# Optimization experiments

Measured on AMD Instinct MI355X. Metric: run time of the kernel, lower is better.

## Reference

```python
import jax, jax.numpy as jnp
import numpy as np

B, N, T, D, H, K = 16, 64, 32, 512, 256, 13
S = N * T  # flattened document length
PAD_TAG = 0


def setup_inputs():
    key = jax.random.key(0)
    ks = jax.random.split(key, 16)
    x = jax.random.normal(ks[0], (B, N, T, D), jnp.float32)
    x_gcn = jax.random.normal(ks[1], (B, N, D), jnp.float32)
    length = jax.random.randint(ks[2], (B, N), 1, T + 1)
    mask = (jnp.arange(T)[None, None, :] < length[:, :, None]).astype(jnp.int32)
    tags = jax.random.randint(ks[3], (B, N, T), 0, K)
    s = 0.05
    w_ih_f = jax.random.normal(ks[4], (4 * H, D), jnp.float32) * s
    w_hh_f = jax.random.normal(ks[5], (4 * H, H), jnp.float32) * s
    b_f = jax.random.normal(ks[6], (4 * H,), jnp.float32) * s
    w_ih_b = jax.random.normal(ks[7], (4 * H, D), jnp.float32) * s
    w_hh_b = jax.random.normal(ks[8], (4 * H, H), jnp.float32) * s
    b_b = jax.random.normal(ks[9], (4 * H,), jnp.float32) * s
    mlp_w = jax.random.normal(ks[10], (K, 2 * H), jnp.float32) * s
    mlp_b = jax.random.normal(ks[11], (K,), jnp.float32) * s
    transitions = jax.random.normal(ks[12], (K, K), jnp.float32) * s
    start_trans = jax.random.normal(ks[13], (K,), jnp.float32) * s
    end_trans = jax.random.normal(ks[14], (K,), jnp.float32) * s
    return dict(x=x, x_gcn=x_gcn, mask=mask, length=length, tags=tags,
                w_ih_f=w_ih_f, w_hh_f=w_hh_f, b_f=b_f,
                w_ih_b=w_ih_b, w_hh_b=w_hh_b, b_b=b_b,
                mlp_w=mlp_w, mlp_b=mlp_b,
                transitions=transitions, start_trans=start_trans, end_trans=end_trans)


def _pack_one(v, dest):
    # scatter valid rows to compacted positions; invalid rows land in dummy slot S
    out = jnp.zeros((S + 1,) + v.shape[1:], v.dtype).at[dest].set(v)
    return out[:S]


def union_layer(x, x_gcn, mask, length, tags):
    xf = x.reshape(B, S, D)
    mf = mask.reshape(B, S)
    tf = tags.reshape(B, S)
    doc_len = length.sum(-1)  # (B,)
    cum = jnp.cumsum(mf, axis=1)
    dest = jnp.where(mf == 1, cum - 1, S)  # invalid -> dummy slot
    new_x = jax.vmap(_pack_one)(xf, dest)
    new_tag = jax.vmap(_pack_one)(tf, dest)  # pad tag = 0
    new_mask = (jnp.arange(S)[None, :] < doc_len[:, None]).astype(mf.dtype)
    gcn_flat = jnp.broadcast_to(x_gcn[:, :, None, :], (B, N, T, D)).reshape(B, S, D)
    return gcn_flat + new_x, new_mask, doc_len, new_tag


def lstm_dir(xs, w_ih, w_hh, b):
    # xs: (B, S, Din) -> hidden states (B, S, H)
    def step(carry, xt):
        h, c = carry
        g = xt @ w_ih.T + h @ w_hh.T + b
        i, f, gg, o = jnp.split(g, 4, axis=-1)
        c = jax.nn.sigmoid(f) * c + jax.nn.sigmoid(i) * jnp.tanh(gg)
        h = jax.nn.sigmoid(o) * jnp.tanh(c)
        return (h, c), h
    init = (jnp.zeros((B, H), xs.dtype), jnp.zeros((B, H), xs.dtype))
    _, hs = jax.lax.scan(step, init, jnp.swapaxes(xs, 0, 1))
    return jnp.swapaxes(hs, 0, 1)


def bilstm(new_x, doc_len, w_ih_f, w_hh_f, b_f, w_ih_b, w_hh_b, b_b):
    t = jnp.arange(S)[None, :]
    L = doc_len[:, None]
    rev = jnp.where(t < L, L - 1 - t, t)  # per-sample reversal within valid region (involution)
    out_f = lstm_dir(new_x, w_ih_f, w_hh_f, b_f)
    x_rev = jnp.take_along_axis(new_x, rev[:, :, None], axis=1)
    out_b = lstm_dir(x_rev, w_ih_b, w_hh_b, b_b)
    out_b = jnp.take_along_axis(out_b, rev[:, :, None], axis=1)
    return jnp.concatenate([out_f, out_b], axis=-1)  # (B, S, 2H)


def crf_log_likelihood(logits, tags, mask, doc_len, transitions, start_trans, end_trans):
    maskf = mask.astype(logits.dtype)
    # numerator: score of the gold path
    emit = jnp.take_along_axis(logits, tags[:, :, None], axis=2)[..., 0]  # (B,S)
    num = start_trans[tags[:, 0]] + (emit * maskf).sum(1)
    tr = transitions[tags[:, :-1], tags[:, 1:]] * maskf[:, 1:]
    num = num + tr.sum(1)
    last_tag = jnp.take_along_axis(tags, (doc_len - 1)[:, None], axis=1)[:, 0]
    num = num + end_trans[last_tag]
    # denominator: forward algorithm
    alpha0 = start_trans[None, :] + logits[:, 0]
    def step(alpha, inp):
        e, m = inp  # (B,K), (B,)
        new = jax.nn.logsumexp(alpha[:, :, None] + transitions[None] + e[:, None, :], axis=1)
        return jnp.where(m[:, None] > 0, new, alpha), None
    alpha, _ = jax.lax.scan(step, alpha0,
                            (jnp.swapaxes(logits[:, 1:], 0, 1), jnp.swapaxes(mask[:, 1:], 0, 1)))
    log_z = jax.nn.logsumexp(alpha + end_trans[None, :], axis=-1)
    return num - log_z  # (B,) per-doc log-likelihood (keepdim=True)


def reference(x, x_gcn, mask, length, tags,
              w_ih_f, w_hh_f, b_f, w_ih_b, w_hh_b, b_b,
              mlp_w, mlp_b, transitions, start_trans, end_trans):
    new_x, new_mask, doc_len, new_tag = union_layer(x, x_gcn, mask, length, tags)
    out = bilstm(new_x, doc_len, w_ih_f, w_hh_f, b_f, w_ih_b, w_hh_b, b_b)
    out = out * new_mask[:, :, None].astype(out.dtype)  # packed-seq padding semantics
    logits = out @ mlp_w.T + mlp_b  # (B, S, K)
    ll = crf_log_likelihood(logits, new_tag, new_mask, doc_len,
                            transitions, start_trans, end_trans)
    return logits, new_mask, ll
```

## Files before the change

kernel.cpp:

```cpp
#include <hip/hip_runtime.h>
#include <hip/hip_fp16.h>
#include <hip/hip_bf16.h>

#define B_ 16
#define N_ 64
#define T_ 32
#define D_ 512
#define H_ 256
#define K_ 13
#define S_ 2048
#define G4_ 1024

typedef float f32x4 __attribute__((ext_vector_type(4)));
typedef short s16x8 __attribute__((ext_vector_type(8)));
typedef int   i32x4 __attribute__((ext_vector_type(4)));

#define INVQ 2.0505324e-5f

#define BAR() do { \
  asm volatile("s_waitcnt lgkmcnt(0)" ::: "memory"); \
  __builtin_amdgcn_s_barrier(); \
  __builtin_amdgcn_sched_barrier(0); \
} while (0)

__device__ __forceinline__ float sigm(float x){ return 1.0f/(1.0f+__expf(-x)); }
__device__ __forceinline__ float tanh_fast(float x){ return 1.0f - 2.0f/(1.0f+__expf(2.0f*x)); }

__global__ void k_prep(const int* __restrict__ length, int* __restrict__ cum, int* __restrict__ doc){
  const int b = threadIdx.x >> 6, n = threadIdx.x & 63;
  const int v = length[b*N_ + n];
  int x = v;
  #pragma unroll
  for (int d = 1; d < 64; d <<= 1){
    int y = __shfl_up(x, d);
    if (n >= d) x += y;
  }
  cum[b*N_ + n] = x - v;
  if (n == 63) doc[b] = x;
}

__global__ __launch_bounds__(256) void k_cast(const float* __restrict__ wf, const float* __restrict__ wb,
                       const float* __restrict__ hf, const float* __restrict__ hb,
                       ushort* __restrict__ wih, signed char* __restrict__ whh8){
  const int i = blockIdx.x*256 + threadIdx.x;
  if (i < 2*G4_*D_){
    const int dir = i / (G4_*D_); const int r = i % (G4_*D_);
    const float v = dir ? wb[r] : wf[r];
    ((__hip_bfloat16*)wih)[i] = __float2bfloat16(v);
  } else {
    const int j2 = i - 2*G4_*D_;
    if (j2 < 2*G4_*H_){
      const int dir = j2 >> 18; const int r = j2 & 262143;
      const float v = (dir ? hb : hf)[r];
      int q = (int)rintf(v * 384.0f);
      whh8[j2] = (signed char)min(127, max(-127, q));
    }
  }
}

__global__ __launch_bounds__(256) void k_srcmap(const int* __restrict__ length, const int* __restrict__ cum,
                         const int* __restrict__ tags, int* __restrict__ src, int* __restrict__ ntag){
  const int i = blockIdx.x*256 + threadIdx.x;
  const int b = i >> 11, nt = i & 2047, n = nt >> 5, t = nt & 31;
  if (t < length[b*N_ + n]){
    const int dest = cum[b*N_ + n] + t;
    src[b*S_ + dest] = nt;
    ntag[b*S_ + dest] = tags[i];
  }
}

__global__ __launch_bounds__(256) void k_newx(const float* __restrict__ x, const float* __restrict__ gcn,
                      const int* __restrict__ src, const int* __restrict__ doc,
                      ushort* __restrict__ nx, float* __restrict__ mask_out){
  const int r = blockIdx.x; const int b = r >> 11, s = r & 2047;
  const int L = doc[b];
  const int d = threadIdx.x*2;
  const float2 g2 = *(const float2*)&gcn[((size_t)(b*N_ + (s>>5)))*D_ + d];
  float v0 = g2.x, v1 = g2.y;
  if (s < L){
    const int nt = src[r];
    const float2 x2 = *(const float2*)&x[((size_t)(b*S_ + nt))*D_ + d];
    v0 += x2.x; v1 += x2.y;
  }
  __hip_bfloat16* o = (__hip_bfloat16*)nx + (size_t)r*D_ + d;
  o[0] = __float2bfloat16(v0); o[1] = __float2bfloat16(v1);
  if (threadIdx.x == 0) mask_out[r] = (s < L) ? 1.0f : 0.0f;
}

__global__ __launch_bounds__(256) void k_gemm(const ushort* __restrict__ A, const ushort* __restrict__ Bw,
    const float* __restrict__ bias_f, const float* __restrict__ bias_b,
    const int* __restrict__ doc, __half* __restrict__ pre){
  const int m0 = blockIdx.x*128, n0 = blockIdx.y*128;
  const int b = m0 >> 11, s0 = m0 & 2047;
  if (s0 >= doc[b]) return;
  __shared__ __align__(16) ushort la[128*40];
  __shared__ __align__(16) ushort lb[128*40];
  const int tid = threadIdx.x, lane = tid & 63, w = tid >> 6;
  const int wr = w >> 1, wc = w & 1;
  const int fr = lane & 15, fq = lane >> 4;
  f32x4 acc[4][4] = {};
  const int srow = tid >> 1;
  const int sko  = (tid & 1)*16;
  for (int kt = 0; kt < 16; ++kt){
    const int k0 = kt*32;
    const float4 a0 = *(const float4*)&A[(size_t)(m0+srow)*512 + k0 + sko];
    const float4 a1 = *(const float4*)&A[(size_t)(m0+srow)*512 + k0 + sko + 8];
    const float4 b0 = *(const float4*)&Bw[(size_t)(n0+srow)*512 + k0 + sko];
    const float4 b1 = *(const float4*)&Bw[(size_t)(n0+srow)*512 + k0 + sko + 8];
    *(float4*)&la[srow*40 + sko]     = a0;
    *(float4*)&la[srow*40 + sko + 8] = a1;
    *(float4*)&lb[srow*40 + sko]     = b0;
    *(float4*)&lb[srow*40 + sko + 8] = b1;
    __syncthreads();
    s16x8 af[4], bfr[4];
    #pragma unroll
    for (int mi=0; mi<4; ++mi) af[mi] = *(const s16x8*)&la[(wr*64+mi*16+fr)*40 + fq*8];
    #pragma unroll
    for (int ni=0; ni<4; ++ni) bfr[ni] = *(const s16x8*)&lb[(wc*64+ni*16+fr)*40 + fq*8];
    #pragma unroll
    for (int mi=0; mi<4; ++mi){
      #pragma unroll
      for (int ni=0; ni<4; ++ni){
        acc[mi][ni] = __builtin_amdgcn_mfma_f32_16x16x32_bf16(af[mi], bfr[ni], acc[mi][ni], 0, 0, 0);
      }
    }
    __syncthreads();
  }
  #pragma unroll
  for (int ni=0; ni<4; ++ni){
    const int n = n0 + wc*64 + ni*16 + fr;
    const float bv = (n < 1024) ? bias_f[n] : bias_b[n-1024];
    #pragma unroll
    for (int mi=0; mi<4; ++mi){
      const int mb = m0 + wr*64 + mi*16 + fq*4;
      #pragma unroll
      for (int j=0; j<4; ++j)
        pre[(size_t)(mb+j)*2048 + n] = __float2half(acc[mi][ni][j] + bv);
    }
  }
}

__global__ __launch_bounds__(512, 2) void k_recur4(
    const signed char* __restrict__ W8,
    const __half* __restrict__ pre, const int* __restrict__ doc,
    float* __restrict__ outh)
{
  const int b = blockIdx.x >> 1, dir = blockIdx.x & 1;
  const int tid = threadIdx.x, lane = tid & 63, wv = tid >> 6;
  const int L = doc[b];

  __shared__ __align__(16) unsigned char hq[2][256];
  __shared__ __align__(16) __half pls[2][1024];

  if (tid < 128) ((unsigned*)hq)[tid] = 0u;

  i32x4 wfrag[2][4][4];
  #pragma unroll
  for (int nt = 0; nt < 2; ++nt)
    #pragma unroll
    for (int g = 0; g < 4; ++g){
      const int row = g*256 + wv*32 + nt*16 + (lane & 15);
      #pragma unroll
      for (int kt = 0; kt < 4; ++kt)
        wfrag[nt][g][kt] = *(const i32x4*)&W8[(size_t)dir*262144 + (size_t)row*256 + kt*64 + (lane>>4)*16];
    }

  auto ldpre = [&](int tt){
    const int pos = dir ? max(L-1-tt, 0) : tt;
    return *(const unsigned*)(pre + ((size_t)(b*S_ + pos))*2048 + dir*1024 + tid*2);
  };

  const unsigned s0v = ldpre(0);
  unsigned f1 = (1 < L) ? ldpre(1) : 0u;
  unsigned f2 = (2 < L) ? ldpre(2) : 0u;
  *(unsigned*)((char*)&pls[0][0] + tid*4) = s0v;
  BAR();

  float cst = 0.f;
  const int u = wv*32 + (lane & 31);
  for (int t = 0; t < L; ++t){
    const int pcur = t & 1, pnxt = pcur ^ 1;
    const int rbuf = (t+1) & 1, wbuf = t & 1;
    const unsigned rn = (t+3 < L) ? ldpre(t+3) : 0u;

    i32x4 af[4] = {{0,0,0,0},{0,0,0,0},{0,0,0,0},{0,0,0,0}};
    if ((lane & 15) == 0){
      #pragma unroll
      for (int kt = 0; kt < 4; ++kt)
        af[kt] = *(const i32x4*)&hq[rbuf][kt*64 + (lane >> 4)*16];
    }
    i32x4 acc[2][4] = {};
    #pragma unroll
    for (int kt = 0; kt < 4; ++kt)
      #pragma unroll
      for (int nt = 0; nt < 2; ++nt)
        #pragma unroll
        for (int g = 0; g < 4; ++g)
          acc[nt][g] = __builtin_amdgcn_mfma_i32_16x16x64_i8(af[kt], wfrag[nt][g][kt], acc[nt][g], 0, 0, 0);

    int ac[4];
    #pragma unroll
    for (int g = 0; g < 4; ++g){
      const int sw = __shfl_xor(acc[1][g][0], 16);
      ac[g] = (lane < 16) ? acc[0][g][0] : sw;
    }
    float hval = 0.f;
    const int pos = dir ? (L-1-t) : t;
    if (lane < 32){
      float gv[4];
      #pragma unroll
      for (int g = 0; g < 4; ++g)
        gv[g] = (float)ac[g]*INVQ + __half2float(pls[pcur][g*256 + u]);
      const float c = sigm(gv[1])*cst + sigm(gv[0])*tanh_fast(gv[2]);
      cst = c;
      hval = sigm(gv[3])*tanh_fast(c);
      outh[((size_t)(b*S_ + pos))*512 + dir*256 + u] = hval;
    }
    int q = (int)rintf(hval*127.0f);
    q = min(127, max(-127, q));
    unsigned v = ((unsigned)(q & 255)) << ((lane & 3)*8);
    v |= __shfl_xor(v, 1);
    v |= __shfl_xor(v, 2);
    if (lane < 32 && (lane & 3) == 0)
      *(unsigned*)&hq[wbuf][u & ~3] = v;
    if (t+1 < L)
      *(unsigned*)((char*)&pls[pnxt][0] + tid*4) = f1;
    f1 = f2; f2 = rn;
    BAR();
  }
}

__global__ __launch_bounds__(256) void k_logits(const float* __restrict__ outh, const float* __restrict__ mw,
    const float* __restrict__ mb, const int* __restrict__ doc, float* __restrict__ logits){
  const int w = threadIdx.x >> 6, lane = threadIdx.x & 63;
  const int r = blockIdx.x*4 + w;
  const int b = r >> 11, s = r & 2047;
  if (s >= doc[b]){
    if (lane < 13) logits[(size_t)r*13 + lane] = mb[lane];
    return;
  }
  float xv[8];
  #pragma unroll
  for (int m=0; m<8; ++m) xv[m] = outh[(size_t)r*512 + lane + m*64];
  #pragma unroll
  for (int k=0; k<13; ++k){
    float p = 0.f;
    #pragma unroll
    for (int m=0; m<8; ++m) p += xv[m]*mw[k*512 + lane + m*64];
    #pragma unroll
    for (int off=32; off; off>>=1) p += __shfl_down(p, off);
    if (lane == 0) logits[(size_t)r*13 + k] = p + mb[k];
  }
}

__global__ void k_crf(const float* __restrict__ logits, const int* __restrict__ ntag,
    const int* __restrict__ doc, const float* __restrict__ trans,
    const float* __restrict__ stt, const float* __restrict__ ent, float* __restrict__ ll){
  const int b = blockIdx.x, lane = threadIdx.x;
  const int L = doc[b];
  const float* lg = logits + (size_t)b*S_*13;
  float tc[13];
  #pragma unroll
  for (int i=0; i<13; ++i) tc[i] = (lane < 13) ? trans[i*13 + lane] : 0.f;
  float alpha = (lane < 13) ? (stt[lane] + lg[lane]) : -1e30f;
  for (int t=1; t<L; ++t){
    const float e = (lane < 13) ? lg[(size_t)t*13 + lane] : 0.f;
    float v[13]; float m = -1e30f;
    #pragma unroll
    for (int i=0; i<13; ++i){ v[i] = __shfl(alpha, i) + tc[i]; m = fmaxf(m, v[i]); }
    float sum = 0.f;
    #pragma unroll
    for (int i=0; i<13; ++i) sum += __expf(v[i] - m);
    alpha = m + __logf(sum) + e;
  }
  float av = (lane < 13) ? alpha + ent[lane] : -1e30f;
  float m2 = -1e30f;
  #pragma unroll
  for (int i=0; i<13; ++i) m2 = fmaxf(m2, __shfl(av, i));
  float s2 = 0.f;
  #pragma unroll
  for (int i=0; i<13; ++i) s2 += __expf(__shfl(av, i) - m2);
  const float logz = m2 + __logf(s2);
  const int* tg = ntag + (size_t)b*S_;
  float num = 0.f;
  for (int t = lane; t < L; t += 64){
    const int cur = tg[t];
    num += lg[(size_t)t*13 + cur];
    if (t >= 1) num += trans[tg[t-1]*13 + cur];
  }
  #pragma unroll
  for (int off=32; off; off>>=1) num += __shfl_down(num, off);
  if (lane == 0){
    num += stt[tg[0]] + ent[tg[L-1]];
    ll[b] = num - logz;
  }
}

extern "C" void kernel_launch(void* const* d_in, const int* in_sizes, int n_in,
                              void* d_out, int out_size, void* d_ws, size_t ws_size,
                              hipStream_t stream){
  const float* x    = (const float*)d_in[0];
  const float* gcn  = (const float*)d_in[1];
  const int* length = (const int*)d_in[3];
  const int* tags   = (const int*)d_in[4];
  const float* wihf = (const float*)d_in[5];
  const float* whhf = (const float*)d_in[6];
  const float* bf   = (const float*)d_in[7];
  const float* wihb = (const float*)d_in[8];
  const float* whhb = (const float*)d_in[9];
  const float* bb   = (const float*)d_in[10];
  const float* mw   = (const float*)d_in[11];
  const float* mb   = (const float*)d_in[12];
  const float* trans= (const float*)d_in[13];
  const float* stt  = (const float*)d_in[14];
  const float* ent  = (const float*)d_in[15];

  char* ws = (char*)d_ws;
  ushort* nx   = (ushort*)(ws + 0);
  __half* pre  = (__half*)(ws + 33554432);
  float*  outh = (float*)(ws + 167772160);
  ushort* wih  = (ushort*)(ws + 234881024);
  signed char* whh8 = (signed char*)(ws + 236978176);
  int*    src  = (int*)(ws + 238026752);
  int*    ntag = (int*)(ws + 238157824);
  int*    cum  = (int*)(ws + 238288896);
  int*    doc  = (int*)(ws + 238292992);

  float* logits  = (float*)d_out;
  float* maskout = logits + 425984;
  float* ll      = maskout + 32768;

  hipLaunchKernelGGL(k_prep,   dim3(1),        dim3(1024), 0, stream, length, cum, doc);
  hipLaunchKernelGGL(k_cast,   dim3(6144),     dim3(256),  0, stream, wihf, wihb, whhf, whhb, wih, whh8);
  hipLaunchKernelGGL(k_srcmap, dim3(128),      dim3(256),  0, stream, length, cum, tags, src, ntag);
  hipLaunchKernelGGL(k_newx,   dim3(32768),    dim3(256),  0, stream, x, gcn, src, doc, nx, maskout);
  hipLaunchKernelGGL(k_gemm,   dim3(256, 16),  dim3(256),  0, stream, nx, wih, bf, bb, doc, pre);
  hipLaunchKernelGGL(k_recur4, dim3(32),       dim3(512),  0, stream, whh8, pre, doc, outh);
  hipLaunchKernelGGL(k_logits, dim3(8192),     dim3(256),  0, stream, outh, mw, mb, doc, logits);
  hipLaunchKernelGGL(k_crf,    dim3(16),       dim3(64),   0, stream, logits, ntag, doc, trans, stt, ent, ll);
}
```

Measured before the change: 1.892 ms.

## Interleave four sequences per recurrence block with ping-pong MFMA/gate overlap

The LSTM recurrence now packs four documents per workgroup (two MFMA row slots per half-step) and alternates two groups so one group's matrix multiply overlaps the other group's gate math, with partial sums exchanged through shared memory. The grid shrinks from 32 to 8 blocks, and each block iterates to the longest of its four documents. Hidden outputs are stored as fp16 instead of fp32, halving write and read traffic for the logits kernel. The cost is padding work up to the block-max length, fewer CUs in use, extra LDS traffic and barriers, and reduced output precision.

```diff
diff --git a/kernel.cpp b/kernel.cpp
--- a/kernel.cpp
+++ b/kernel.cpp
@@ -140,97 +140,157 @@
   }
 }
 
-__global__ __launch_bounds__(512, 2) void k_recur4(
+__global__ __launch_bounds__(512, 2) void k_recur5(
     const signed char* __restrict__ W8,
     const __half* __restrict__ pre, const int* __restrict__ doc,
-    float* __restrict__ outh)
+    __half* __restrict__ outh)
 {
-  const int b = blockIdx.x >> 1, dir = blockIdx.x & 1;
+  const int q = blockIdx.x >> 1, dir = blockIdx.x & 1;
   const int tid = threadIdx.x, lane = tid & 63, wv = tid >> 6;
-  const int L = doc[b];
-
-  __shared__ __align__(16) unsigned char hq[2][256];
-  __shared__ __align__(16) __half pls[2][1024];
-
-  if (tid < 128) ((unsigned*)hq)[tid] = 0u;
+  const int fr = lane & 15;
+  const int cl = lane >> 5;
+  const int ul = lane & 31;
+  const int u  = wv*32 + ul;
+
+  __shared__ __align__(16) signed char hq[2][2][2][256];
+  __shared__ __align__(16) int rsc[8][4][32][2];
+
+  ((unsigned*)hq)[tid] = 0u;
+
+  const int b1 = q*4 + cl;
+  const int b2 = q*4 + 2 + cl;
+  const int L1 = doc[b1], L2 = doc[b2];
+  int Lblk = 0;
+  #pragma unroll
+  for (int j = 0; j < 4; ++j) Lblk = max(Lblk, doc[q*4+j]);
 
   i32x4 wfrag[2][4][4];
   #pragma unroll
   for (int nt = 0; nt < 2; ++nt)
     #pragma unroll
     for (int g = 0; g < 4; ++g){
-      const int row = g*256 + wv*32 + nt*16 + (lane & 15);
+      const int row = g*256 + wv*32 + nt*16 + fr;
       #pragma unroll
       for (int kt = 0; kt < 4; ++kt)
         wfrag[nt][g][kt] = *(const i32x4*)&W8[(size_t)dir*262144 + (size_t)row*256 + kt*64 + (lane>>4)*16];
     }
 
-  auto ldpre = [&](int tt){
-    const int pos = dir ? max(L-1-tt, 0) : tt;
-    return *(const unsigned*)(pre + ((size_t)(b*S_ + pos))*2048 + dir*1024 + tid*2);
-  };
-
-  const unsigned s0v = ldpre(0);
-  unsigned f1 = (1 < L) ? ldpre(1) : 0u;
-  unsigned f2 = (2 < L) ? ldpre(2) : 0u;
-  *(unsigned*)((char*)&pls[0][0] + tid*4) = s0v;
+  i32x4 af[4]  = {{0,0,0,0},{0,0,0,0},{0,0,0,0},{0,0,0,0}};
+  i32x4 accA[2][4] = {};
+  i32x4 accB[2][4] = {};
+
+  const __half* pb1 = pre + (size_t)b1*S_*2048 + dir*1024 + u;
+  const __half* pb2 = pre + (size_t)b2*S_*2048 + dir*1024 + u;
+  __half* ob1 = outh + (size_t)b1*S_*512 + dir*256 + u;
+  __half* ob2 = outh + (size_t)b2*S_*512 + dir*256 + u;
+
+  float c1s = 0.f, c2s = 0.f;
   BAR();
 
-  float cst = 0.f;
-  const int u = wv*32 + (lane & 31);
-  for (int t = 0; t < L; ++t){
-    const int pcur = t & 1, pnxt = pcur ^ 1;
-    const int rbuf = (t+1) & 1, wbuf = t & 1;
-    const unsigned rn = (t+3 < L) ? ldpre(t+3) : 0u;
-
-    i32x4 af[4] = {{0,0,0,0},{0,0,0,0},{0,0,0,0},{0,0,0,0}};
-    if ((lane & 15) == 0){
+  for (int t = 0; t < Lblk; ++t){
+    const int buf = t & 1, nbuf = buf ^ 1;
+    const int pos1 = dir ? max(L1-1-t, 0) : t;
+    const int pos2 = dir ? max(L2-1-t, 0) : t;
+
+    __half pg1[4], pg2[4];
+    {
+      const __half* p2 = pb2 + (size_t)pos2*2048;
+      const __half* p1 = pb1 + (size_t)pos1*2048;
+      #pragma unroll
+      for (int g = 0; g < 4; ++g) pg2[g] = p2[g*256];
+      #pragma unroll
+      for (int g = 0; g < 4; ++g) pg1[g] = p1[g*256];
+    }
+
+    if (fr < 2){
       #pragma unroll
       for (int kt = 0; kt < 4; ++kt)
-        af[kt] = *(const i32x4*)&hq[rbuf][kt*64 + (lane >> 4)*16];
-    }
-    i32x4 acc[2][4] = {};
+        af[kt] = *(const i32x4*)&hq[0][buf][fr][kt*64 + (lane>>4)*16];
+    }
     #pragma unroll
     for (int kt = 0; kt < 4; ++kt)
       #pragma unroll
       for (int nt = 0; nt < 2; ++nt)
         #pragma unroll
         for (int g = 0; g < 4; ++g)
-          acc[nt][g] = __builtin_amdgcn_mfma_i32_16x16x64_i8(af[kt], wfrag[nt][g][kt], acc[nt][g], 0, 0, 0);
-
-    int ac[4];
-    #pragma unroll
-    for (int g = 0; g < 4; ++g){
-      const int sw = __shfl_xor(acc[1][g][0], 16);
-      ac[g] = (lane < 16) ? acc[0][g][0] : sw;
-    }
-    float hval = 0.f;
-    const int pos = dir ? (L-1-t) : t;
-    if (lane < 32){
+          accA[nt][g] = __builtin_amdgcn_mfma_i32_16x16x64_i8(af[kt], wfrag[nt][g][kt], accA[nt][g], 0, 0, 0);
+
+    if (lane < 16){
+      #pragma unroll
+      for (int nt = 0; nt < 2; ++nt)
+        #pragma unroll
+        for (int g = 0; g < 4; ++g){
+          int2 v; v.x = accB[nt][g][0]; v.y = accB[nt][g][1];
+          *(int2*)&rsc[wv][g][nt*16 + fr][0] = v;
+        }
+    }
+    #pragma unroll
+    for (int nt = 0; nt < 2; ++nt)
+      #pragma unroll
+      for (int g = 0; g < 4; ++g)
+        accB[nt][g] = (i32x4){0,0,0,0};
+
+    {
       float gv[4];
       #pragma unroll
       for (int g = 0; g < 4; ++g)
-        gv[g] = (float)ac[g]*INVQ + __half2float(pls[pcur][g*256 + u]);
-      const float c = sigm(gv[1])*cst + sigm(gv[0])*tanh_fast(gv[2]);
-      cst = c;
-      hval = sigm(gv[3])*tanh_fast(c);
-      outh[((size_t)(b*S_ + pos))*512 + dir*256 + u] = hval;
-    }
-    int q = (int)rintf(hval*127.0f);
-    q = min(127, max(-127, q));
-    unsigned v = ((unsigned)(q & 255)) << ((lane & 3)*8);
-    v |= __shfl_xor(v, 1);
-    v |= __shfl_xor(v, 2);
-    if (lane < 32 && (lane & 3) == 0)
-      *(unsigned*)&hq[wbuf][u & ~3] = v;
-    if (t+1 < L)
-      *(unsigned*)((char*)&pls[pnxt][0] + tid*4) = f1;
-    f1 = f2; f2 = rn;
+        gv[g] = (float)rsc[wv][g][ul][cl]*INVQ + __half2float(pg2[g]);
+      const float c = sigm(gv[1])*c2s + sigm(gv[0])*tanh_fast(gv[2]);
+      c2s = c;
+      const float h = sigm(gv[3])*tanh_fast(c);
+      int q8 = (int)rintf(h*127.0f);
+      q8 = min(127, max(-127, q8));
+      hq[1][nbuf][cl][u] = (signed char)q8;
+      if (t < L2) ob2[(size_t)pos2*512] = __float2half(h);
+    }
     BAR();
-  }
-}
-
-__global__ __launch_bounds__(256) void k_logits(const float* __restrict__ outh, const float* __restrict__ mw,
+
+    if (fr < 2){
+      #pragma unroll
+      for (int kt = 0; kt < 4; ++kt)
+        af[kt] = *(const i32x4*)&hq[1][nbuf][fr][kt*64 + (lane>>4)*16];
+    }
+    #pragma unroll
+    for (int kt = 0; kt < 4; ++kt)
+      #pragma unroll
+      for (int nt = 0; nt < 2; ++nt)
+        #pragma unroll
+        for (int g = 0; g < 4; ++g)
+          accB[nt][g] = __builtin_amdgcn_mfma_i32_16x16x64_i8(af[kt], wfrag[nt][g][kt], accB[nt][g], 0, 0, 0);
+
+    if (lane < 16){
+      #pragma unroll
+      for (int nt = 0; nt < 2; ++nt)
+        #pragma unroll
+        for (int g = 0; g < 4; ++g){
+          int2 v; v.x = accA[nt][g][0]; v.y = accA[nt][g][1];
+          *(int2*)&rsc[wv][g][nt*16 + fr][0] = v;
+        }
+    }
+    #pragma unroll
+    for (int nt = 0; nt < 2; ++nt)
+      #pragma unroll
+      for (int g = 0; g < 4; ++g)
+        accA[nt][g] = (i32x4){0,0,0,0};
+
+    {
+      float gv[4];
+      #pragma unroll
+      for (int g = 0; g < 4; ++g)
+        gv[g] = (float)rsc[wv][g][ul][cl]*INVQ + __half2float(pg1[g]);
+      const float c = sigm(gv[1])*c1s + sigm(gv[0])*tanh_fast(gv[2]);
+      c1s = c;
+      const float h = sigm(gv[3])*tanh_fast(c);
+      int q8 = (int)rintf(h*127.0f);
+      q8 = min(127, max(-127, q8));
+      hq[0][nbuf][cl][u] = (signed char)q8;
+      if (t < L1) ob1[(size_t)pos1*512] = __float2half(h);
+    }
+    BAR();
+  }
+}
+
+__global__ __launch_bounds__(256) void k_logits(const __half* __restrict__ outh, const float* __restrict__ mw,
     const float* __restrict__ mb, const int* __restrict__ doc, float* __restrict__ logits){
   const int w = threadIdx.x >> 6, lane = threadIdx.x & 63;
   const int r = blockIdx.x*4 + w;
@@ -241,7 +301,7 @@
   }
   float xv[8];
   #pragma unroll
-  for (int m=0; m<8; ++m) xv[m] = outh[(size_t)r*512 + lane + m*64];
+  for (int m=0; m<8; ++m) xv[m] = __half2float(outh[(size_t)r*512 + lane + m*64]);
   #pragma unroll
   for (int k=0; k<13; ++k){
     float p = 0.f;
@@ -318,7 +378,7 @@
   char* ws = (char*)d_ws;
   ushort* nx   = (ushort*)(ws + 0);
   __half* pre  = (__half*)(ws + 33554432);
-  float*  outh = (float*)(ws + 167772160);
+  __half* outh = (__half*)(ws + 167772160);
   ushort* wih  = (ushort*)(ws + 234881024);
   signed char* whh8 = (signed char*)(ws + 236978176);
   int*    src  = (int*)(ws + 238026752);
@@ -335,7 +395,7 @@
   hipLaunchKernelGGL(k_srcmap, dim3(128),      dim3(256),  0, stream, length, cum, tags, src, ntag);
   hipLaunchKernelGGL(k_newx,   dim3(32768),    dim3(256),  0, stream, x, gcn, src, doc, nx, maskout);
   hipLaunchKernelGGL(k_gemm,   dim3(256, 16),  dim3(256),  0, stream, nx, wih, bf, bb, doc, pre);
-  hipLaunchKernelGGL(k_recur4, dim3(32),       dim3(512),  0, stream, whh8, pre, doc, outh);
+  hipLaunchKernelGGL(k_recur5, dim3(8),        dim3(512),  0, stream, whh8, pre, doc, outh);
   hipLaunchKernelGGL(k_logits, dim3(8192),     dim3(256),  0, stream, outh, mw, mb, doc, logits);
   hipLaunchKernelGGL(k_crf,    dim3(16),       dim3(64),   0, stream, logits, ntag, doc, trans, stt, ent, ll);
 }
```

New measurement: 2.909 ms. +53.7%, slower.

## Interleave gate preactivations per unit, store LSTM outputs as fp16, simplify CRF step

Applied to the files above, without the earlier changes.

The GEMM epilogue now writes preactivations interleaved as [unit][gate], so each recurrence lane fetches its four gate values with one 8-byte load a step ahead. This removes the shared-memory staging buffer and its extra store per step. LSTM hidden outputs are stored as fp16 to cut write and read traffic for the logits kernel, at some precision cost. The CRF forward step now uses exp(transitions) with a single max-shift per step instead of 13 exponentials per lane.

```diff
diff --git a/kernel.cpp b/kernel.cpp
--- a/kernel.cpp
+++ b/kernel.cpp
@@ -130,27 +130,28 @@
   for (int ni=0; ni<4; ++ni){
     const int n = n0 + wc*64 + ni*16 + fr;
     const float bv = (n < 1024) ? bias_f[n] : bias_b[n-1024];
+    const int dir = n >> 10, g = (n >> 8) & 3, u = n & 255;
+    const int col = dir*1024 + u*4 + g;
     #pragma unroll
     for (int mi=0; mi<4; ++mi){
       const int mb = m0 + wr*64 + mi*16 + fq*4;
       #pragma unroll
       for (int j=0; j<4; ++j)
-        pre[(size_t)(mb+j)*2048 + n] = __float2half(acc[mi][ni][j] + bv);
-    }
-  }
-}
-
-__global__ __launch_bounds__(512, 2) void k_recur4(
+        pre[(size_t)(mb+j)*2048 + col] = __float2half(acc[mi][ni][j] + bv);
+    }
+  }
+}
+
+__global__ __launch_bounds__(512, 2) void k_recur10(
     const signed char* __restrict__ W8,
     const __half* __restrict__ pre, const int* __restrict__ doc,
-    float* __restrict__ outh)
+    __half* __restrict__ outh)
 {
   const int b = blockIdx.x >> 1, dir = blockIdx.x & 1;
   const int tid = threadIdx.x, lane = tid & 63, wv = tid >> 6;
   const int L = doc[b];
 
-  __shared__ __align__(16) unsigned char hq[2][256];
-  __shared__ __align__(16) __half pls[2][1024];
+  __shared__ __align__(16) signed char hq[2][256];
 
   if (tid < 128) ((unsigned*)hq)[tid] = 0u;
 
@@ -165,23 +166,23 @@
         wfrag[nt][g][kt] = *(const i32x4*)&W8[(size_t)dir*262144 + (size_t)row*256 + kt*64 + (lane>>4)*16];
     }
 
-  auto ldpre = [&](int tt){
-    const int pos = dir ? max(L-1-tt, 0) : tt;
-    return *(const unsigned*)(pre + ((size_t)(b*S_ + pos))*2048 + dir*1024 + tid*2);
-  };
-
-  const unsigned s0v = ldpre(0);
-  unsigned f1 = (1 < L) ? ldpre(1) : 0u;
-  unsigned f2 = (2 < L) ? ldpre(2) : 0u;
-  *(unsigned*)((char*)&pls[0][0] + tid*4) = s0v;
+  const int u = wv*32 + (lane & 31);
+  const int pos0 = dir ? (L-1) : 0;
+  const __half* pp = pre + ((size_t)(b*S_ + pos0))*2048 + dir*1024 + u*4;
+  __half*       op = outh + ((size_t)(b*S_ + pos0))*512 + dir*256 + u;
+  const ptrdiff_t dp  = dir ? -2048 : 2048;
+  const ptrdiff_t dph = dir ? -512  : 512;
+
+  float cst = 0.f;
+  uint2 pv = {0,0}, pvn = {0,0};
+  if (lane < 32) pv = *(const uint2*)pp;
   BAR();
 
-  float cst = 0.f;
-  const int u = wv*32 + (lane & 31);
   for (int t = 0; t < L; ++t){
-    const int pcur = t & 1, pnxt = pcur ^ 1;
+    if (lane < 32 && t+1 < L) pvn = *(const uint2*)(pp + dp);
+    pp += dp;
+
     const int rbuf = (t+1) & 1, wbuf = t & 1;
-    const unsigned rn = (t+3 < L) ? ldpre(t+3) : 0u;
 
     i32x4 af[4] = {{0,0,0,0},{0,0,0,0},{0,0,0,0},{0,0,0,0}};
     if ((lane & 15) == 0){
@@ -205,17 +206,20 @@
       ac[g] = (lane < 16) ? acc[0][g][0] : sw;
     }
     float hval = 0.f;
-    const int pos = dir ? (L-1-t) : t;
     if (lane < 32){
-      float gv[4];
-      #pragma unroll
-      for (int g = 0; g < 4; ++g)
-        gv[g] = (float)ac[g]*INVQ + __half2float(pls[pcur][g*256 + u]);
-      const float c = sigm(gv[1])*cst + sigm(gv[0])*tanh_fast(gv[2]);
+      const __half2* ph = (const __half2*)&pv;
+      const float2 p01 = __half22float2(ph[0]);
+      const float2 p23 = __half22float2(ph[1]);
+      const float gi = (float)ac[0]*INVQ + p01.x;
+      const float gf = (float)ac[1]*INVQ + p01.y;
+      const float gg = (float)ac[2]*INVQ + p23.x;
+      const float go = (float)ac[3]*INVQ + p23.y;
+      const float c = sigm(gf)*cst + sigm(gi)*tanh_fast(gg);
       cst = c;
-      hval = sigm(gv[3])*tanh_fast(c);
-      outh[((size_t)(b*S_ + pos))*512 + dir*256 + u] = hval;
-    }
+      hval = sigm(go)*tanh_fast(c);
+      *op = __float2half(hval);
+    }
+    op += dph;
     int q = (int)rintf(hval*127.0f);
     q = min(127, max(-127, q));
     unsigned v = ((unsigned)(q & 255)) << ((lane & 3)*8);
@@ -223,14 +227,12 @@
     v |= __shfl_xor(v, 2);
     if (lane < 32 && (lane & 3) == 0)
       *(unsigned*)&hq[wbuf][u & ~3] = v;
-    if (t+1 < L)
-      *(unsigned*)((char*)&pls[pnxt][0] + tid*4) = f1;
-    f1 = f2; f2 = rn;
+    pv = pvn;
     BAR();
   }
 }
 
-__global__ __launch_bounds__(256) void k_logits(const float* __restrict__ outh, const float* __restrict__ mw,
+__global__ __launch_bounds__(256) void k_logits(const __half* __restrict__ outh, const float* __restrict__ mw,
     const float* __restrict__ mb, const int* __restrict__ doc, float* __restrict__ logits){
   const int w = threadIdx.x >> 6, lane = threadIdx.x & 63;
   const int r = blockIdx.x*4 + w;
@@ -241,7 +243,7 @@
   }
   float xv[8];
   #pragma unroll
-  for (int m=0; m<8; ++m) xv[m] = outh[(size_t)r*512 + lane + m*64];
+  for (int m=0; m<8; ++m) xv[m] = __half2float(outh[(size_t)r*512 + lane + m*64]);
   #pragma unroll
   for (int k=0; k<13; ++k){
     float p = 0.f;
@@ -259,19 +261,22 @@
   const int b = blockIdx.x, lane = threadIdx.x;
   const int L = doc[b];
   const float* lg = logits + (size_t)b*S_*13;
-  float tc[13];
-  #pragma unroll
-  for (int i=0; i<13; ++i) tc[i] = (lane < 13) ? trans[i*13 + lane] : 0.f;
+  float et[13];
+  #pragma unroll
+  for (int i=0; i<13; ++i) et[i] = (lane < 13) ? __expf(trans[i*13 + lane]) : 0.f;
   float alpha = (lane < 13) ? (stt[lane] + lg[lane]) : -1e30f;
+  float e_nxt = (L > 1 && lane < 13) ? lg[13 + lane] : 0.f;
   for (int t=1; t<L; ++t){
-    const float e = (lane < 13) ? lg[(size_t)t*13 + lane] : 0.f;
-    float v[13]; float m = -1e30f;
-    #pragma unroll
-    for (int i=0; i<13; ++i){ v[i] = __shfl(alpha, i) + tc[i]; m = fmaxf(m, v[i]); }
-    float sum = 0.f;
-    #pragma unroll
-    for (int i=0; i<13; ++i) sum += __expf(v[i] - m);
-    alpha = m + __logf(sum) + e;
+    const float e = e_nxt;
+    if (t+1 < L && lane < 13) e_nxt = lg[(size_t)(t+1)*13 + lane];
+    float m = alpha;
+    #pragma unroll
+    for (int off = 1; off < 16; off <<= 1) m = fmaxf(m, __shfl_xor(m, off));
+    const float a = __expf(alpha - m);
+    float s = 0.f;
+    #pragma unroll
+    for (int i=0; i<13; ++i) s += __shfl(a, i) * et[i];
+    alpha = m + __logf(s) + e;
   }
   float av = (lane < 13) ? alpha + ent[lane] : -1e30f;
   float m2 = -1e30f;
@@ -318,7 +323,7 @@
   char* ws = (char*)d_ws;
   ushort* nx   = (ushort*)(ws + 0);
   __half* pre  = (__half*)(ws + 33554432);
-  float*  outh = (float*)(ws + 167772160);
+  __half* outh = (__half*)(ws + 167772160);
   ushort* wih  = (ushort*)(ws + 234881024);
   signed char* whh8 = (signed char*)(ws + 236978176);
   int*    src  = (int*)(ws + 238026752);
@@ -335,7 +340,7 @@
   hipLaunchKernelGGL(k_srcmap, dim3(128),      dim3(256),  0, stream, length, cum, tags, src, ntag);
   hipLaunchKernelGGL(k_newx,   dim3(32768),    dim3(256),  0, stream, x, gcn, src, doc, nx, maskout);
   hipLaunchKernelGGL(k_gemm,   dim3(256, 16),  dim3(256),  0, stream, nx, wih, bf, bb, doc, pre);
-  hipLaunchKernelGGL(k_recur4, dim3(32),       dim3(512),  0, stream, whh8, pre, doc, outh);
+  hipLaunchKernelGGL(k_recur10, dim3(32),      dim3(512),  0, stream, whh8, pre, doc, outh);
   hipLaunchKernelGGL(k_logits, dim3(8192),     dim3(256),  0, stream, outh, mw, mb, doc, logits);
   hipLaunchKernelGGL(k_crf,    dim3(16),       dim3(64),   0, stream, logits, ntag, doc, trans, stt, ent, ll);
 }
```

Result: faster. 1.799 ms (-4.9%).
